# Kernel optimization log

Hardware: AMD Instinct MI355X
Metric: run time of the kernel (lower is better)

Reference implementation:

```python
import jax, jax.numpy as jnp
import numpy as np
import math

B, C_IN, N_SEL, N_DROP, HEADS = 4, 128, 1024, 1024, 4
Q_OUT = K_OUT = V_OUT = 256
N = N_SEL + N_DROP


def setup_inputs() -> dict:
    key = jax.random.key(0)
    ks = jax.random.split(key, 8)
    pcd_up = jax.random.normal(ks[0], (B, C_IN, N), jnp.float32)
    points_select = jax.random.normal(ks[1], (B, C_IN, N_SEL), jnp.float32)
    points_drop = jax.random.normal(ks[2], (B, C_IN, N_DROP), jnp.float32)
    # per-batch permutation of [0, N) split into select/drop halves (collision-free scatter)
    perms = jax.vmap(lambda k: jax.random.permutation(k, N))(jax.random.split(ks[3], B))
    idx_select = perms[:, None, :N_SEL].astype(jnp.int32)
    idx_drop = perms[:, None, N_SEL:].astype(jnp.int32)
    scale = 1.0 / math.sqrt(C_IN)
    Wq = jax.random.normal(ks[4], (Q_OUT, C_IN), jnp.float32) * scale
    Wk = jax.random.normal(ks[5], (K_OUT, C_IN), jnp.float32) * scale
    Wv = jax.random.normal(ks[6], (V_OUT, C_IN), jnp.float32) * scale
    Wskip = jax.random.normal(ks[7], (V_OUT, C_IN), jnp.float32) * scale
    return {"pcd_up": pcd_up, "points_select": points_select, "points_drop": points_drop,
            "idx_select": idx_select, "idx_drop": idx_drop,
            "Wq": Wq, "Wk": Wk, "Wv": Wv, "Wskip": Wskip}


def _concat_by_idx(a, b, idx_a, idx_b):
    # scatter columns of concat([a,b]) to positions given by concat([idx_a, idx_b])
    src = jnp.concatenate([a, b], axis=-1)            # (B, C, N)
    idx = jnp.concatenate([idx_a, idx_b], axis=-1)[:, 0, :]  # (B, N)
    return jax.vmap(lambda s, i: jnp.zeros_like(s).at[:, i].set(s))(src, idx)


def reference(pcd_up, points_select, points_drop, idx_select, idx_drop, Wq, Wk, Wv, Wskip):
    b, _, n = pcd_up.shape
    x = _concat_by_idx(points_select, points_drop, idx_select, idx_drop)  # (B, C_in, N)
    # 1x1 convs (no bias) == channel matmuls, then split heads: (B, H, D, N)
    q = jnp.einsum('oc,bcn->bon', Wq, x).reshape(b, HEADS, Q_OUT // HEADS, n)
    k = jnp.einsum('oc,bcn->bon', Wk, x).reshape(b, HEADS, K_OUT // HEADS, n)
    v = jnp.einsum('oc,bcn->bon', Wv, x).reshape(b, HEADS, V_OUT // HEADS, n)
    energy = jnp.einsum('bhdn,bhdm->bhnm', q, k)      # (B, H, N, N)
    attn = jax.nn.softmax(energy / math.sqrt(Q_OUT // HEADS), axis=-1)
    out = jnp.einsum('bhnm,bhdm->bhnd', attn, v)      # (B, H, N, Dv)
    out = out.transpose(0, 2, 1, 3).reshape(b, n, V_OUT).transpose(0, 2, 1)  # (B, V_out, N)
    skip = jnp.einsum('oc,bcn->bon', Wskip, pcd_up)   # (B, V_out, N)
    return skip + out
```

## Files before the change

### kernel.cpp

```cpp
#include <hip/hip_runtime.h>
#include <hip/hip_bf16.h>
#include <math.h>

#define B_    4
#define C_IN_ 128
#define N_    2048
#define NSEL_ 1024
#define H_    4
#define KS_   4

typedef __bf16 bf16;
typedef __bf16 bf16x2 __attribute__((ext_vector_type(2)));
typedef __bf16 bf16x4 __attribute__((ext_vector_type(4)));
typedef __bf16 bf16x8 __attribute__((ext_vector_type(8)));
typedef float  f32x4  __attribute__((ext_vector_type(4)));

__device__ __forceinline__ void gll16(const void* g, void* l) {
    __builtin_amdgcn_global_load_lds((const __attribute__((address_space(1))) void*)g,
                                     (__attribute__((address_space(3))) void*)l,
                                     16, 0, 0);
}

__device__ __forceinline__ float fast_exp2(float x) {
#if __has_builtin(__builtin_amdgcn_exp2f)
    return __builtin_amdgcn_exp2f(x);
#else
    return exp2f(x);
#endif
}

__global__ __launch_bounds__(256) void prep_kernel(
    const int* __restrict__ isel, const int* __restrict__ idrp,
    const float* __restrict__ Wq, const float* __restrict__ Wk,
    const float* __restrict__ Wv, const float* __restrict__ Ws,
    int* __restrict__ inv, bf16* __restrict__ Wbf)
{
    const int blk = blockIdx.x;
    if (blk < 128) {
        int e = blk * 256 + threadIdx.x;
        int which = e >> 13, idx = e & 8191;
        const float* Wx = (which == 0) ? Wq : (which == 1) ? Wk
                        : (which == 2) ? Wv : Ws;
        float4 v = *(const float4*)(Wx + (size_t)idx * 4);
        bf16x4 o; o[0] = (bf16)v.x; o[1] = (bf16)v.y; o[2] = (bf16)v.z; o[3] = (bf16)v.w;
        *(bf16x4*)(Wbf + (size_t)which * 32768 + (size_t)idx * 4) = o;
    } else {
        int g = (blk - 128) * 256 + threadIdx.x;
        int b = g >> 11, j = g & (N_ - 1);
        int pos = (j < NSEL_) ? isel[b * NSEL_ + j] : idrp[b * NSEL_ + (j - NSEL_)];
        inv[b * N_ + (pos & (N_ - 1))] = j;
    }
}

#define XSTR 136

__global__ __launch_bounds__(256) void qkv_mfma_kernel(
    const float* __restrict__ sel, const float* __restrict__ drop,
    const bf16* __restrict__ Wbf,
    bf16* __restrict__ qT, bf16* __restrict__ kTt, bf16* __restrict__ vTt)
{
    const int ntile = blockIdx.x;
    const int which = blockIdx.y >> 1;
    const int rh    = blockIdx.y & 1;
    const int b     = blockIdx.z;
    const int tid   = threadIdx.x;
    const int w     = tid >> 6;
    const int lane  = tid & 63;
    const int quad  = lane >> 4;
    const int lc    = lane & 15;
    const int n0    = ntile * 64;

    __shared__ __align__(16) bf16 xT[64 * XSTR];

    const float* srcp; int rstride;
    if (ntile < 16) { srcp = sel  + (size_t)b * C_IN_ * NSEL_ + n0;           rstride = NSEL_; }
    else            { srcp = drop + (size_t)b * C_IN_ * NSEL_ + (n0 - NSEL_); rstride = NSEL_; }

    #pragma unroll
    for (int k = 0; k < 4; ++k) {
        int e  = tid + k * 256;
        int cp = e >> 4, nq = e & 15;
        int c0 = cp * 2;
        float4 v0 = *(const float4*)(srcp + (size_t)c0 * rstride + nq * 4);
        float4 v1 = *(const float4*)(srcp + (size_t)(c0 + 1) * rstride + nq * 4);
        int cc = c0 ^ ((nq & 3) << 3);
        float a0[4] = {v0.x, v0.y, v0.z, v0.w};
        float a1[4] = {v1.x, v1.y, v1.z, v1.w};
        #pragma unroll
        for (int i = 0; i < 4; ++i) {
            int n = nq * 4 + i;
            bf16x2 t; t[0] = (bf16)a0[i]; t[1] = (bf16)a1[i];
            *(bf16x2*)&xT[n * XSTR + cc] = t;
        }
    }
    __syncthreads();

    const bf16* wbase = Wbf + (size_t)which * 256 * 128;
    const int rbase = rh * 128 + w * 32;

    f32x4 acc[8];
    #pragma unroll
    for (int i = 0; i < 8; ++i) acc[i] = (f32x4){0.f, 0.f, 0.f, 0.f};

    #pragma unroll
    for (int kq = 0; kq < 4; ++kq) {
        bf16x8 wf[2], xA[4];
        #pragma unroll
        for (int ot = 0; ot < 2; ++ot)
            wf[ot] = *(const bf16x8*)(wbase + (size_t)(rbase + ot * 16 + lc) * 128 + kq * 32 + quad * 8);
        #pragma unroll
        for (int nt = 0; nt < 4; ++nt) {
            int row = nt * 16 + lc;
            int col = (kq * 32 + quad * 8) ^ (((row >> 2) & 3) << 3);
            xA[nt] = *(const bf16x8*)&xT[row * XSTR + col];
        }
        if (which <= 1) {
            #pragma unroll
            for (int nt = 0; nt < 4; ++nt)
                #pragma unroll
                for (int ot = 0; ot < 2; ++ot)
                    acc[nt * 2 + ot] = __builtin_amdgcn_mfma_f32_16x16x32_bf16(xA[nt], wf[ot], acc[nt * 2 + ot], 0, 0, 0);
        } else {
            #pragma unroll
            for (int ot = 0; ot < 2; ++ot)
                #pragma unroll
                for (int nt = 0; nt < 4; ++nt)
                    acc[ot * 4 + nt] = __builtin_amdgcn_mfma_f32_16x16x32_bf16(wf[ot], xA[nt], acc[ot * 4 + nt], 0, 0, 0);
        }
    }

    if (which <= 1) {
        #pragma unroll
        for (int nt = 0; nt < 4; ++nt) {
            #pragma unroll
            for (int ot = 0; ot < 2; ++ot) {
                #pragma unroll
                for (int r = 0; r < 4; ++r) {
                    int n    = n0 + nt * 16 + quad * 4 + r;
                    int rloc = nt * 16 + quad * 4 + r;
                    int o256 = rbase + ot * 16 + lc;
                    int h = o256 >> 6, d = o256 & 63;
                    float val = acc[nt * 2 + ot][r];
                    if (which == 0)
                        qT[((size_t)(b * H_ + h) * N_ + n) * 64 + d] = (bf16)(val * 0.18033688011f);
                    else
                        kTt[(((size_t)(b * H_ + h) * 32 + ntile) << 12) | (rloc << 6) | (d ^ ((rloc & 7) << 3))] = (bf16)val;
                }
            }
        }
    } else {
        #pragma unroll
        for (int ot = 0; ot < 2; ++ot) {
            #pragma unroll
            for (int r = 0; r < 4; ++r) {
                int o256 = rbase + ot * 16 + quad * 4 + r;
                int h = o256 >> 6, dv = o256 & 63;
                bf16x4 pk;
                #pragma unroll
                for (int nt = 0; nt < 4; ++nt) pk[nt] = (bf16)acc[ot * 4 + nt][r];
                int scol = (lc * 4) ^ ((dv & 7) << 3);
                *(bf16x4*)(vTt + ((((size_t)(b * H_ + h) * 32 + ntile) << 12) | (dv << 6) | scol)) = pk;
            }
        }
    }
}

#define PSTR 72

__global__ __launch_bounds__(256, 2) void attn_kernel(
    const bf16* __restrict__ qT, const bf16* __restrict__ kTt,
    const bf16* __restrict__ vTt, bf16* __restrict__ Opart,
    float* __restrict__ S_ws)
{
    const int id    = blockIdx.x;
    const int bh    = (id & 7) + 8 * ((id >> 3) & 1);
    const int qb    = (id >> 4) & 7;
    const int c     = id >> 7;
    const int b     = bh >> 2;
    const int h     = bh & 3;
    const int tid   = threadIdx.x;
    const int w     = tid >> 6;
    const int lane  = tid & 63;
    const int quad  = lane >> 4;
    const int lc    = lane & 15;
    const int n0    = qb * 256 + w * 64;

    __shared__ __align__(16) bf16 sK[2][64 * 64];
    __shared__ __align__(16) bf16 sV[2][64 * 64];
    __shared__ __align__(16) bf16 p_lds[4 * 16 * PSTR];
    bf16* pw = &p_lds[w * 16 * PSTR];

    const bf16* kbase = kTt + (((size_t)bh * 32 + c * 8) << 12);
    const bf16* vbase = vTt + (((size_t)bh * 32 + c * 8) << 12);

    #pragma unroll
    for (int j = 0; j < 2; ++j) {
        const int sseg = (w * 2 + j) << 9;
        gll16(kbase + sseg + lane * 8, &sK[0][sseg]);
        gll16(vbase + sseg + lane * 8, &sV[0][sseg]);
    }

    bf16x8 aq[4][2];
    #pragma unroll
    for (int t = 0; t < 4; ++t) {
        const bf16* qp = qT + ((size_t)bh * N_ + n0 + t * 16 + lc) * 64 + quad * 8;
        aq[t][0] = *(const bf16x8*)(qp);
        aq[t][1] = *(const bf16x8*)(qp + 32);
    }

    f32x4 accO[4][4];
    #pragma unroll
    for (int t = 0; t < 4; ++t)
        #pragma unroll
        for (int i = 0; i < 4; ++i) accO[t][i] = (f32x4){0.f, 0.f, 0.f, 0.f};
    float psum[4][4] = {{0.f,0.f,0.f,0.f},{0.f,0.f,0.f,0.f},
                        {0.f,0.f,0.f,0.f},{0.f,0.f,0.f,0.f}};

    const int rswz = (lc & 7) << 3;

    for (int s = 0; s < 8; ++s) {
        const int buf = s & 1;
        __syncthreads();

        if (s < 7) {
            const bf16* kg = kbase + ((size_t)(s + 1) << 12);
            const bf16* vg = vbase + ((size_t)(s + 1) << 12);
            #pragma unroll
            for (int j = 0; j < 2; ++j) {
                const int sseg = (w * 2 + j) << 9;
                gll16(kg + sseg + lane * 8, &sK[buf ^ 1][sseg]);
                gll16(vg + sseg + lane * 8, &sV[buf ^ 1][sseg]);
            }
        }

        bf16x8 kf[4][2], vf[4][2];
        #pragma unroll
        for (int mt = 0; mt < 4; ++mt) {
            const int rb = (mt * 16 + lc) * 64;
            kf[mt][0] = *(const bf16x8*)&sK[buf][rb + ((quad * 8) ^ rswz)];
            kf[mt][1] = *(const bf16x8*)&sK[buf][rb + ((quad * 8 + 32) ^ rswz)];
            vf[mt][0] = *(const bf16x8*)&sV[buf][rb + ((quad * 8) ^ rswz)];
            vf[mt][1] = *(const bf16x8*)&sV[buf][rb + ((quad * 8 + 32) ^ rswz)];
        }

        #pragma unroll
        for (int t = 0; t < 4; ++t) {
            f32x4 accS[4];
            #pragma unroll
            for (int mt = 0; mt < 4; ++mt) {
                f32x4 z = (f32x4){0.f, 0.f, 0.f, 0.f};
                z = __builtin_amdgcn_mfma_f32_16x16x32_bf16(aq[t][0], kf[mt][0], z, 0, 0, 0);
                z = __builtin_amdgcn_mfma_f32_16x16x32_bf16(aq[t][1], kf[mt][1], z, 0, 0, 0);
                accS[mt] = z;
            }
            #pragma unroll
            for (int r = 0; r < 4; ++r) {
                float sum = 0.f;
                #pragma unroll
                for (int mt = 0; mt < 4; ++mt) {
                    float p = fast_exp2(accS[mt][r]);
                    accS[mt][r] = p;
                    sum += p;
                }
                psum[t][r] += sum;
            }
            #pragma unroll
            for (int r = 0; r < 4; ++r) {
                bf16x4 pk;
                #pragma unroll
                for (int mt = 0; mt < 4; ++mt) pk[mt] = (bf16)accS[mt][r];
                *(bf16x4*)&pw[(quad * 4 + r) * PSTR + lc * 4] = pk;
            }
            bf16x8 ap0 = *(const bf16x8*)(&pw[lc * PSTR + quad * 8]);
            bf16x8 ap1 = *(const bf16x8*)(&pw[lc * PSTR + 32 + quad * 8]);
            #pragma unroll
            for (int dvt = 0; dvt < 4; ++dvt) {
                accO[t][dvt] = __builtin_amdgcn_mfma_f32_16x16x32_bf16(ap0, vf[dvt][0], accO[t][dvt], 0, 0, 0);
                accO[t][dvt] = __builtin_amdgcn_mfma_f32_16x16x32_bf16(ap1, vf[dvt][1], accO[t][dvt], 0, 0, 0);
            }
        }
    }

    #pragma unroll
    for (int t = 0; t < 4; ++t) {
        float inv_[4];
        #pragma unroll
        for (int r = 0; r < 4; ++r) {
            float s = psum[t][r];
            #pragma unroll
            for (int off = 1; off < 16; off <<= 1)
                s += __shfl_xor(s, off, 64);
            inv_[r] = 1.f / s;
            int n = n0 + t * 16 + quad * 4 + r;
            if (lc == 0)
                S_ws[((size_t)(c * B_ + b) * H_ + h) * N_ + n] = s;
        }
        #pragma unroll
        for (int r = 0; r < 4; ++r) {
            int n = n0 + t * 16 + quad * 4 + r;
            #pragma unroll
            for (int dvt = 0; dvt < 4; ++dvt) {
                int o = h * 64 + dvt * 16 + lc;
                Opart[((size_t)(c * B_ + b) * N_ + n) * 256 + o] = (bf16)(accO[t][dvt][r] * inv_[r]);
            }
        }
    }
}

__global__ __launch_bounds__(256) void scatter_kernel(
    const bf16* __restrict__ Opart, const float* __restrict__ S_ws,
    const int* __restrict__ inv, const float* __restrict__ pcd,
    const bf16* __restrict__ Wbf, float* __restrict__ out)
{
    const int ptile = blockIdx.x;
    const int og    = blockIdx.y;
    const int b     = blockIdx.z;
    const int tid   = threadIdx.x;
    const int w     = tid >> 6;
    const int lane  = tid & 63;
    const int quad  = lane >> 4;
    const int lc    = lane & 15;
    const int p0    = ptile * 64;

    __shared__ __align__(16) bf16 xT[64 * XSTR];
    __shared__ __align__(16) bf16 lds[64 * 72];

    const int row0 = tid >> 3, seg = tid & 7, row1 = row0 + 32;
    int j0 = inv[b * N_ + p0 + row0] & (N_ - 1);
    int j1 = inv[b * N_ + p0 + row1] & (N_ - 1);
    float sv0[KS_], sv1[KS_];
    bf16x8 g0[KS_], g1[KS_];
    #pragma unroll
    for (int cc = 0; cc < KS_; ++cc) {
        g0[cc] = *(const bf16x8*)(Opart + (((size_t)(cc * B_ + b) * N_ + j0) << 8) + og * 64 + seg * 8);
        g1[cc] = *(const bf16x8*)(Opart + (((size_t)(cc * B_ + b) * N_ + j1) << 8) + og * 64 + seg * 8);
        sv0[cc] = S_ws[((size_t)(cc * B_ + b) * H_ + og) * N_ + j0];
        sv1[cc] = S_ws[((size_t)(cc * B_ + b) * H_ + og) * N_ + j1];
    }

    const float* srcp = pcd + (size_t)b * C_IN_ * N_ + p0;
    #pragma unroll
    for (int k = 0; k < 4; ++k) {
        int e  = tid + k * 256;
        int cp = e >> 4, nq = e & 15;
        int c0 = cp * 2;
        float4 v0 = *(const float4*)(srcp + (size_t)c0 * N_ + nq * 4);
        float4 v1 = *(const float4*)(srcp + (size_t)(c0 + 1) * N_ + nq * 4);
        int cc = c0 ^ ((nq & 3) << 3);
        float a0[4] = {v0.x, v0.y, v0.z, v0.w};
        float a1[4] = {v1.x, v1.y, v1.z, v1.w};
        #pragma unroll
        for (int i = 0; i < 4; ++i) {
            int n = nq * 4 + i;
            bf16x2 t; t[0] = (bf16)a0[i]; t[1] = (bf16)a1[i];
            *(bf16x2*)&xT[n * XSTR + cc] = t;
        }
    }
    __syncthreads();

    const bf16* wbase = Wbf + (size_t)3 * 256 * 128 + (size_t)(og * 64 + w * 16) * 128;
    f32x4 acc[4];
    #pragma unroll
    for (int i = 0; i < 4; ++i) acc[i] = (f32x4){0.f, 0.f, 0.f, 0.f};
    #pragma unroll
    for (int kq = 0; kq < 4; ++kq) {
        bf16x8 A = *(const bf16x8*)(wbase + (size_t)lc * 128 + kq * 32 + quad * 8);
        #pragma unroll
        for (int nt = 0; nt < 4; ++nt) {
            int row = nt * 16 + lc;
            int col = (kq * 32 + quad * 8) ^ (((row >> 2) & 3) << 3);
            bf16x8 Bf = *(const bf16x8*)&xT[row * XSTR + col];
            acc[nt] = __builtin_amdgcn_mfma_f32_16x16x32_bf16(A, Bf, acc[nt], 0, 0, 0);
        }
    }

    {
        float d0 = 0.f, d1 = 0.f;
        #pragma unroll
        for (int cc = 0; cc < KS_; ++cc) { d0 += sv0[cc]; d1 += sv1[cc]; }
        float id0 = 1.f / d0, id1 = 1.f / d1;
        float a8[8], b8[8];
        #pragma unroll
        for (int i = 0; i < 8; ++i) { a8[i] = 0.f; b8[i] = 0.f; }
        #pragma unroll
        for (int cc = 0; cc < KS_; ++cc) {
            float w0 = sv0[cc] * id0, w1 = sv1[cc] * id1;
            #pragma unroll
            for (int i = 0; i < 8; ++i) {
                a8[i] += w0 * (float)g0[cc][i];
                b8[i] += w1 * (float)g1[cc][i];
            }
        }
        bf16x8 o8, p8;
        #pragma unroll
        for (int i = 0; i < 8; ++i) { o8[i] = (bf16)a8[i]; p8[i] = (bf16)b8[i]; }
        *(bf16x8*)&lds[row0 * 72 + seg * 8] = o8;
        *(bf16x8*)&lds[row1 * 72 + seg * 8] = p8;
    }
    __syncthreads();

    #pragma unroll
    for (int nt = 0; nt < 4; ++nt) {
        #pragma unroll
        for (int r = 0; r < 4; ++r) {
            int o_loc = w * 16 + quad * 4 + r;
            int p     = nt * 16 + lc;
            float attn = (float)lds[p * 72 + o_loc];
            out[((size_t)b * 256 + og * 64 + o_loc) * N_ + p0 + p] = acc[nt][r] + attn;
        }
    }
}

extern "C" void kernel_launch(void* const* d_in, const int* in_sizes, int n_in,
                              void* d_out, int out_size, void* d_ws, size_t ws_size,
                              hipStream_t stream) {
    const float* pcd  = (const float*)d_in[0];
    const float* sel  = (const float*)d_in[1];
    const float* drop = (const float*)d_in[2];
    const int*   isel = (const int*)d_in[3];
    const int*   idrp = (const int*)d_in[4];
    const float* Wq   = (const float*)d_in[5];
    const float* Wk   = (const float*)d_in[6];
    const float* Wv   = (const float*)d_in[7];
    const float* Ws   = (const float*)d_in[8];
    float* out = (float*)d_out;

    const size_t MB = 1024 * 1024;
    char*  ws    = (char*)d_ws;
    bf16*  qT    = (bf16*)(ws);
    bf16*  kTt   = (bf16*)(ws + 4 * MB);
    bf16*  vTt   = (bf16*)(ws + 8 * MB);
    bf16*  Opart = (bf16*)(ws + 12 * MB);
    float* S_ws  = (float*)(ws + 28 * MB);
    bf16*  Wbf   = (bf16*)(ws + 28 * MB + 512 * 1024);
    int*   inv   = (int*)(ws + 28 * MB + 768 * 1024);

    prep_kernel<<<dim3(160), 256, 0, stream>>>(isel, idrp, Wq, Wk, Wv, Ws, inv, Wbf);
    qkv_mfma_kernel<<<dim3(32, 6, B_), 256, 0, stream>>>(sel, drop, Wbf,
                                                         qT, kTt, vTt);
    attn_kernel<<<dim3(16 * 8 * KS_), 256, 0, stream>>>(qT, kTt, vTt, Opart, S_ws);
    scatter_kernel<<<dim3(32, 4, B_), 256, 0, stream>>>(Opart, S_ws, inv, pcd, Wbf, out);
}
```

Baseline: 117.8 us.

## Move skip projection into QKV kernel and stage K stores through LDS

The Wskip projection of pcd_up moves from the scatter kernel into the QKV kernel as a fourth 'which' group, which writes the skip result straight into the output buffer. The scatter kernel then only does a float4 read-modify-write that adds the attention result. The skip GEMM now runs alongside the independent QKV work instead of sitting in the tail kernel after attention. K outputs are also transposed through LDS so they can be written as 16-byte vector stores instead of scalar stores. The cost is an extra output read in the scatter kernel and more blocks in the QKV launch.

```diff
diff --git a/kernel.cpp b/kernel.cpp
--- a/kernel.cpp
+++ b/kernel.cpp
@@ -55,9 +55,10 @@
 #define XSTR 136
 
 __global__ __launch_bounds__(256) void qkv_mfma_kernel(
-    const float* __restrict__ sel, const float* __restrict__ drop,
-    const bf16* __restrict__ Wbf,
-    bf16* __restrict__ qT, bf16* __restrict__ kTt, bf16* __restrict__ vTt)
+    const float* __restrict__ pcd, const float* __restrict__ sel,
+    const float* __restrict__ drop, const bf16* __restrict__ Wbf,
+    bf16* __restrict__ qT, bf16* __restrict__ kTt, bf16* __restrict__ vTt,
+    float* __restrict__ out)
 {
     const int ntile = blockIdx.x;
     const int which = blockIdx.y >> 1;
@@ -73,8 +74,9 @@
     __shared__ __align__(16) bf16 xT[64 * XSTR];
 
     const float* srcp; int rstride;
-    if (ntile < 16) { srcp = sel  + (size_t)b * C_IN_ * NSEL_ + n0;           rstride = NSEL_; }
-    else            { srcp = drop + (size_t)b * C_IN_ * NSEL_ + (n0 - NSEL_); rstride = NSEL_; }
+    if (which == 3)      { srcp = pcd + (size_t)b * C_IN_ * N_ + n0;          rstride = N_; }
+    else if (ntile < 16) { srcp = sel  + (size_t)b * C_IN_ * NSEL_ + n0;      rstride = NSEL_; }
+    else                 { srcp = drop + (size_t)b * C_IN_ * NSEL_ + (n0 - NSEL_); rstride = NSEL_; }
 
     #pragma unroll
     for (int k = 0; k < 4; ++k) {
@@ -129,7 +131,7 @@
         }
     }
 
-    if (which <= 1) {
+    if (which == 0) {
         #pragma unroll
         for (int nt = 0; nt < 4; ++nt) {
             #pragma unroll
@@ -137,18 +139,39 @@
                 #pragma unroll
                 for (int r = 0; r < 4; ++r) {
                     int n    = n0 + nt * 16 + quad * 4 + r;
-                    int rloc = nt * 16 + quad * 4 + r;
                     int o256 = rbase + ot * 16 + lc;
                     int h = o256 >> 6, d = o256 & 63;
-                    float val = acc[nt * 2 + ot][r];
-                    if (which == 0)
-                        qT[((size_t)(b * H_ + h) * N_ + n) * 64 + d] = (bf16)(val * 0.18033688011f);
-                    else
-                        kTt[(((size_t)(b * H_ + h) * 32 + ntile) << 12) | (rloc << 6) | (d ^ ((rloc & 7) << 3))] = (bf16)val;
+                    qT[((size_t)(b * H_ + h) * N_ + n) * 64 + d] =
+                        (bf16)(acc[nt * 2 + ot][r] * 0.18033688011f);
                 }
             }
         }
-    } else {
+    } else if (which == 1) {
+        __syncthreads();
+        #pragma unroll
+        for (int nt = 0; nt < 4; ++nt) {
+            #pragma unroll
+            for (int ot = 0; ot < 2; ++ot) {
+                #pragma unroll
+                for (int r = 0; r < 4; ++r) {
+                    int rloc = nt * 16 + quad * 4 + r;
+                    int ol   = w * 32 + ot * 16 + lc;
+                    xT[rloc * XSTR + ol] = (bf16)acc[nt * 2 + ot][r];
+                }
+            }
+        }
+        __syncthreads();
+        const int ol8 = (lane & 15) * 8;
+        const int h0  = rh * 2 + (ol8 >> 6);
+        const int d0  = ol8 & 63;
+        #pragma unroll
+        for (int i = 0; i < 4; ++i) {
+            int row = w * 16 + (lane >> 4) * 4 + i;
+            bf16x8 v = *(const bf16x8*)&xT[row * XSTR + ol8];
+            *(bf16x8*)(kTt + ((((size_t)(b * H_ + h0) * 32 + ntile) << 12)
+                              | (row << 6) | (d0 ^ ((row & 7) << 3)))) = v;
+        }
+    } else if (which == 2) {
         #pragma unroll
         for (int ot = 0; ot < 2; ++ot) {
             #pragma unroll
@@ -160,6 +183,18 @@
                 for (int nt = 0; nt < 4; ++nt) pk[nt] = (bf16)acc[ot * 4 + nt][r];
                 int scol = (lc * 4) ^ ((dv & 7) << 3);
                 *(bf16x4*)(vTt + ((((size_t)(b * H_ + h) * 32 + ntile) << 12) | (dv << 6) | scol)) = pk;
+            }
+        }
+    } else {
+        #pragma unroll
+        for (int ot = 0; ot < 2; ++ot) {
+            #pragma unroll
+            for (int r = 0; r < 4; ++r) {
+                int o256 = rbase + ot * 16 + quad * 4 + r;
+                float* orow = out + ((size_t)b * 256 + o256) * N_ + n0;
+                #pragma unroll
+                for (int nt = 0; nt < 4; ++nt)
+                    orow[nt * 16 + lc] = acc[ot * 4 + nt][r];
             }
         }
     }
@@ -309,20 +344,14 @@
 
 __global__ __launch_bounds__(256) void scatter_kernel(
     const bf16* __restrict__ Opart, const float* __restrict__ S_ws,
-    const int* __restrict__ inv, const float* __restrict__ pcd,
-    const bf16* __restrict__ Wbf, float* __restrict__ out)
+    const int* __restrict__ inv, float* __restrict__ out)
 {
     const int ptile = blockIdx.x;
     const int og    = blockIdx.y;
     const int b     = blockIdx.z;
     const int tid   = threadIdx.x;
-    const int w     = tid >> 6;
-    const int lane  = tid & 63;
-    const int quad  = lane >> 4;
-    const int lc    = lane & 15;
     const int p0    = ptile * 64;
 
-    __shared__ __align__(16) bf16 xT[64 * XSTR];
     __shared__ __align__(16) bf16 lds[64 * 72];
 
     const int row0 = tid >> 3, seg = tid & 7, row1 = row0 + 32;
@@ -338,42 +367,6 @@
         sv1[cc] = S_ws[((size_t)(cc * B_ + b) * H_ + og) * N_ + j1];
     }
 
-    const float* srcp = pcd + (size_t)b * C_IN_ * N_ + p0;
-    #pragma unroll
-    for (int k = 0; k < 4; ++k) {
-        int e  = tid + k * 256;
-        int cp = e >> 4, nq = e & 15;
-        int c0 = cp * 2;
-        float4 v0 = *(const float4*)(srcp + (size_t)c0 * N_ + nq * 4);
-        float4 v1 = *(const float4*)(srcp + (size_t)(c0 + 1) * N_ + nq * 4);
-        int cc = c0 ^ ((nq & 3) << 3);
-        float a0[4] = {v0.x, v0.y, v0.z, v0.w};
-        float a1[4] = {v1.x, v1.y, v1.z, v1.w};
-        #pragma unroll
-        for (int i = 0; i < 4; ++i) {
-            int n = nq * 4 + i;
-            bf16x2 t; t[0] = (bf16)a0[i]; t[1] = (bf16)a1[i];
-            *(bf16x2*)&xT[n * XSTR + cc] = t;
-        }
-    }
-    __syncthreads();
-
-    const bf16* wbase = Wbf + (size_t)3 * 256 * 128 + (size_t)(og * 64 + w * 16) * 128;
-    f32x4 acc[4];
-    #pragma unroll
-    for (int i = 0; i < 4; ++i) acc[i] = (f32x4){0.f, 0.f, 0.f, 0.f};
-    #pragma unroll
-    for (int kq = 0; kq < 4; ++kq) {
-        bf16x8 A = *(const bf16x8*)(wbase + (size_t)lc * 128 + kq * 32 + quad * 8);
-        #pragma unroll
-        for (int nt = 0; nt < 4; ++nt) {
-            int row = nt * 16 + lc;
-            int col = (kq * 32 + quad * 8) ^ (((row >> 2) & 3) << 3);
-            bf16x8 Bf = *(const bf16x8*)&xT[row * XSTR + col];
-            acc[nt] = __builtin_amdgcn_mfma_f32_16x16x32_bf16(A, Bf, acc[nt], 0, 0, 0);
-        }
-    }
-
     {
         float d0 = 0.f, d1 = 0.f;
         #pragma unroll
@@ -399,15 +392,18 @@
     }
     __syncthreads();
 
-    #pragma unroll
-    for (int nt = 0; nt < 4; ++nt) {
-        #pragma unroll
-        for (int r = 0; r < 4; ++r) {
-            int o_loc = w * 16 + quad * 4 + r;
-            int p     = nt * 16 + lc;
-            float attn = (float)lds[p * 72 + o_loc];
-            out[((size_t)b * 256 + og * 64 + o_loc) * N_ + p0 + p] = acc[nt][r] + attn;
-        }
+    const int o_loc = tid >> 2;
+    const int i4    = tid & 3;
+    float* orow = out + ((size_t)b * 256 + og * 64 + o_loc) * N_ + p0;
+    #pragma unroll
+    for (int k = 0; k < 4; ++k) {
+        int p = k * 16 + i4 * 4;
+        float4 v = *(float4*)(orow + p);
+        v.x += (float)lds[(p + 0) * 72 + o_loc];
+        v.y += (float)lds[(p + 1) * 72 + o_loc];
+        v.z += (float)lds[(p + 2) * 72 + o_loc];
+        v.w += (float)lds[(p + 3) * 72 + o_loc];
+        *(float4*)(orow + p) = v;
     }
 }
 
@@ -436,8 +432,8 @@
     int*   inv   = (int*)(ws + 28 * MB + 768 * 1024);
 
     prep_kernel<<<dim3(160), 256, 0, stream>>>(isel, idrp, Wq, Wk, Wv, Ws, inv, Wbf);
-    qkv_mfma_kernel<<<dim3(32, 6, B_), 256, 0, stream>>>(sel, drop, Wbf,
-                                                         qT, kTt, vTt);
+    qkv_mfma_kernel<<<dim3(32, 8, B_), 256, 0, stream>>>(pcd, sel, drop, Wbf,
+                                                         qT, kTt, vTt, out);
     attn_kernel<<<dim3(16 * 8 * KS_), 256, 0, stream>>>(qT, kTt, vTt, Opart, S_ws);
-    scatter_kernel<<<dim3(32, 4, B_), 256, 0, stream>>>(Opart, S_ws, inv, pcd, Wbf, out);
-}
+    scatter_kernel<<<dim3(32, 4, B_), 256, 0, stream>>>(Opart, S_ws, inv, out);
+}
```

New measurement: 120.4 us. 1.02x slower.
